# Optimization experiments

Hardware: AMD Instinct MI355X
Metric: run time of the kernel (lower is better)

Reference implementation:

```python
import jax, jax.numpy as jnp
import numpy as np

B, S, L = 2, 1024, 1024
DIM_Q, H, K, D_C, D_CQ, R = 2048, 16, 128, 512, 1536, 64


def _rope_tables(length, dim):
    # matches _RoPECache._build_tables: repeat_interleave(2) layout
    inv = 1.0 / (10000.0 ** (jnp.arange(0, dim, 2, dtype=jnp.float32) / dim))
    f = jnp.arange(length, dtype=jnp.float32)[:, None] * inv[None, :]  # [len, dim/2]
    sin = jnp.repeat(jnp.sin(f), 2, axis=-1)
    cos = jnp.repeat(jnp.cos(f), 2, axis=-1)
    return sin, cos


def _rotate_half(x):
    half = x.shape[-1] // 2
    return jnp.concatenate([-x[..., half:], x[..., :half]], axis=-1)


def _apply_rope(x, sin, cos):
    return x * cos + _rotate_half(x) * sin


def setup_inputs() -> dict:
    key = jax.random.key(0)
    ks = jax.random.split(key, 8)
    return {
        "hidden_q": jax.random.normal(ks[0], (B, S, DIM_Q), jnp.float32),
        "kv_c": jax.random.normal(ks[1], (B, L, D_C), jnp.float32),
        "Wq": jax.random.normal(ks[2], (H * K, DIM_Q), jnp.float32) / np.sqrt(DIM_Q).astype(np.float32),
        "w_kc_q": jax.random.normal(ks[3], (H, K, D_CQ), jnp.float32) / np.sqrt(K).astype(np.float32),
        "w_kc_kv": jax.random.normal(ks[4], (H, K, D_C), jnp.float32) / np.sqrt(K).astype(np.float32),
        "W_qr": jax.random.normal(ks[5], (H, D_CQ, R), jnp.float32) / np.float32(np.sqrt(D_CQ) * np.sqrt(R)),
        "W_kr": jax.random.normal(ks[6], (H, D_C, R), jnp.float32) / np.sqrt(D_C).astype(np.float32),
        "Wo": jax.random.normal(ks[7], (DIM_Q, H * K), jnp.float32) / np.sqrt(H * K).astype(np.float32),
    }


def reference(hidden_q, kv_c, Wq, w_kc_q, w_kc_kv, W_qr, W_kr, Wo):
    Bv, Sv, _ = hidden_q.shape
    _, Lv, _ = kv_c.shape
    # latent -> per-head queries, then decompress to d_cq
    q_hk = (hidden_q @ Wq.T).reshape(Bv, Sv, H, K)          # [B,S,H,K]
    q_big = jnp.einsum('bshk,hkq->bshq', q_hk, w_kc_q)      # [B,S,H,d_cq]
    sin_q, cos_q = _rope_tables(Sv, D_CQ)
    q_big = _apply_rope(q_big, sin_q[None, :, None, :], cos_q[None, :, None, :])
    sin_k, cos_k = _rope_tables(Lv, D_C)
    kv_r = _apply_rope(kv_c, sin_k[None], cos_k[None])      # [B,L,d_c]
    # retrieval projections (scale 1/sqrt(r) baked into W_qr)
    q_r = jnp.einsum('bshq,hqr->bhsr', q_big, W_qr)         # [B,H,S,r]
    k_r = jnp.einsum('bld,hdr->bhlr', kv_r, W_kr)           # [B,H,L,r]
    scores = jnp.einsum('bhsr,bhlr->bhsl', q_r, k_r)
    attn = jax.nn.softmax(scores, axis=-1)
    # values are the (RoPE'd) compressed kv shared across heads
    ctx_c = jnp.einsum('bhsl,bld->bhsd', attn, kv_r)        # [B,H,S,d_c]
    # decompress context: w_kc_kv.transpose(1,2) is [H,d_c,K]
    ctx_lat = jnp.einsum('bhsd,hkd->bhsk', ctx_c, w_kc_kv)  # [B,H,S,K]
    ctx = ctx_lat.transpose(0, 2, 1, 3).reshape(Bv, Sv, H * K)
    return ctx @ Wo.T
```

## Files before the change

kernel.cpp:

```cpp
#include <hip/hip_runtime.h>
#include <hip/hip_bf16.h>


typedef __attribute__((ext_vector_type(8))) short short8;
typedef __attribute__((ext_vector_type(4))) float f32x4;

__device__ __forceinline__ unsigned short f2bs(float v){
  __hip_bfloat16 b = __float2bfloat16(v);
  return *reinterpret_cast<unsigned short*>(&b);
}
__device__ __forceinline__ void storeC(float* p, float v){ *p = v; }
__device__ __forceinline__ void storeC(unsigned short* p, float v){ *p = f2bs(v); }

__device__ __forceinline__ void gl_lds16(const void* g, void* l){
  __builtin_amdgcn_global_load_lds(
      (const __attribute__((address_space(1))) unsigned int*)g,
      (__attribute__((address_space(3))) unsigned int*)l, 16, 0, 0);
}

template<int N> __device__ __forceinline__ void wait_vmcnt(){
  if constexpr (N==0)       asm volatile("s_waitcnt vmcnt(0)" ::: "memory");
  else if constexpr (N==3)  asm volatile("s_waitcnt vmcnt(3)" ::: "memory");
  else if constexpr (N==4)  asm volatile("s_waitcnt vmcnt(4)" ::: "memory");
  else if constexpr (N==6)  asm volatile("s_waitcnt vmcnt(6)" ::: "memory");
  else if constexpr (N==8)  asm volatile("s_waitcnt vmcnt(8)" ::: "memory");
  else if constexpr (N==14) asm volatile("s_waitcnt vmcnt(14)" ::: "memory");
  else if constexpr (N==16) asm volatile("s_waitcnt vmcnt(16)" ::: "memory");
  else if constexpr (N==22) asm volatile("s_waitcnt vmcnt(22)" ::: "memory");
  else static_assert(N==0, "unsupported vmcnt");
}

__device__ __forceinline__ void transpose_tile(
    const float* ip, unsigned short* op, int R, int Cn, int c0, int r0)
{
  __shared__ float tile[32][33];
  int tr = threadIdx.x>>5, tc = threadIdx.x&31;
  #pragma unroll
  for (int i=0;i<4;i++)
    tile[tr+i*8][tc] = ip[(long)(r0+tr+i*8)*Cn + c0+tc];
  __syncthreads();
  #pragma unroll
  for (int i=0;i<4;i++)
    op[(long)(c0+tr+i*8)*R + r0+tc] = f2bs(tile[tc][tr+i*8]);
}

__global__ __launch_bounds__(256) void prep_all(
    float4* __restrict__ rq,
    const float* __restrict__ kvc, unsigned short* __restrict__ kvrb,
    const float* __restrict__ hidden, unsigned short* __restrict__ hiddenb,
    const float* __restrict__ Wq, unsigned short* __restrict__ Wqb,
    const float* __restrict__ wkckv, unsigned short* __restrict__ wkckvb,
    const float* __restrict__ Wo, unsigned short* __restrict__ Wob,
    const float* __restrict__ wkcq, unsigned short* __restrict__ wkcqT,
    const float* __restrict__ Wqr, unsigned short* __restrict__ WqrT,
    const float* __restrict__ Wkr, unsigned short* __restrict__ WkrT)
{
  int blk = blockIdx.x;
  if (blk < 3072){
    int idx = blk*256 + threadIdx.x;
    int s = idx / 768, j = idx - (idx/768)*768;
    int i1 = j >> 1;
    const float cst = -0.011992631f;
    float f1 = (float)s * __expf(cst * (float)i1);
    float f2 = (float)s * __expf(cst * (float)(384 + i1));
    float s1, c1, s2, c2;
    __sincosf(f1, &s1, &c1);
    __sincosf(f2, &s2, &c2);
    rq[idx] = make_float4(c1, s1, c2, s2);
    return;
  }
  if (blk < 4096){
    int idx = (blk-3072)*256 + threadIdx.x;
    int i1 = idx & 127;
    int l  = (idx >> 7) & 1023;
    int bb = idx >> 17;
    const float cst = -0.035977892f;
    float f1 = (float)l * __expf(cst * (float)i1);
    float f2 = (float)l * __expf(cst * (float)(128 + i1));
    float s1,c1,s2,c2; __sincosf(f1,&s1,&c1); __sincosf(f2,&s2,&c2);
    long base = ((long)bb*1024 + l)*512;
    float2 xlo = *(const float2*)&kvc[base + 2*i1];
    float2 xhi = *(const float2*)&kvc[base + 2*i1 + 256];
    unsigned int lo = (unsigned)f2bs(xlo.x*c1 - xhi.x*s1)
                    | ((unsigned)f2bs(xlo.y*c1 - xhi.y*s1) << 16);
    unsigned int hi = (unsigned)f2bs(xhi.x*c2 + xlo.x*s2)
                    | ((unsigned)f2bs(xhi.y*c2 + xlo.y*s2) << 16);
    *(unsigned int*)&kvrb[base + 2*i1]       = lo;
    *(unsigned int*)&kvrb[base + 2*i1 + 256] = hi;
    return;
  }
  if (blk < 17408){
    const float* in; unsigned short* out; int i;
    if (blk < 8192){ in = hidden; out = hiddenb; i = (blk-4096)*256 + threadIdx.x; }
    else if (blk < 12288){ in = Wq; out = Wqb; i = (blk-8192)*256 + threadIdx.x; }
    else if (blk < 13312){ in = wkckv; out = wkckvb; i = (blk-12288)*256 + threadIdx.x; }
    else { in = Wo; out = Wob; i = (blk-13312)*256 + threadIdx.x; }
    float4 v = *(const float4*)(in + (long)i*4);
    ushort4 u; u.x=f2bs(v.x); u.y=f2bs(v.y); u.z=f2bs(v.z); u.w=f2bs(v.w);
    *(ushort4*)(out + (long)i*4) = u;
    return;
  }
  if (blk < 20480){
    int b2 = blk - 17408;
    int x = b2 % 48, rem = b2 / 48, y = rem % 4, z = rem >> 2;
    transpose_tile(wkcq + (long)z*196608, wkcqT + (long)z*196608,
                   128, 1536, x*32, y*32);
    return;
  }
  if (blk < 22016){
    int b2 = blk - 20480;
    int x = b2 & 1, rem = b2 >> 1, y = rem % 48, z = rem / 48;
    transpose_tile(Wqr + (long)z*98304, WqrT + (long)z*98304,
                   1536, 64, x*32, y*32);
    return;
  }
  {
    int b2 = blk - 22016;
    int x = b2 & 1, y = (b2 >> 1) & 15, z = b2 >> 5;
    transpose_tile(Wkr + (long)z*32768, WkrT + (long)z*32768,
                   512, 64, x*32, y*32);
  }
}

template<int BM,int BN,int WM,int WN,typename TC>
__global__ __launch_bounds__(256) void gemm_mfma(
    const unsigned short* __restrict__ A, const unsigned short* __restrict__ B,
    TC* __restrict__ C,
    int Kd, int lda, int ldb, int ldc, int Hb,
    long sAb, long sAh, long sBb, long sBh, long sCb, long sCh)
{
  constexpr int MF = WM/16, NF = WN/16;
  constexpr int WGM = BM/WM;
  constexpr int AOPS = (4*BM)/256;
  constexpr int BOPS = (4*BN)/256;
  constexpr int STG  = AOPS + BOPS;

  const int z = blockIdx.z, bb = z/Hb, hh = z - bb*Hb;
  const unsigned short* Ap = A + bb*sAb + hh*sAh;
  const unsigned short* Bp = B + bb*sBb + hh*sBh;
  TC* Cp = C + bb*sCb + hh*sCh;
  const int m0 = blockIdx.x*BM, n0 = blockIdx.y*BN;
  const int t = threadIdx.x, w = t>>6, l = t&63;
  const int wm0 = (w % WGM)*WM, wn0 = (w / WGM)*WN;
  const int lq = l>>4, lm = l&15;

  __shared__ __align__(16) unsigned short As[4][4*BM*8];
  __shared__ __align__(16) unsigned short Bs[4][4*BN*8];

  f32x4 acc[MF][NF];
  #pragma unroll
  for (int mf=0; mf<MF; ++mf)
    #pragma unroll
    for (int nf=0; nf<NF; ++nf)
      acc[mf][nf] = f32x4{0.f,0.f,0.f,0.f};

  auto stage = [&](int buf, int k0){
    #pragma unroll
    for (int o = 0; o < AOPS; ++o){
      int g = o*256 + t;
      int row = g & (BM-1), kq = g / BM;
      gl_lds16(Ap + (long)(m0+row)*lda + k0 + kq*8, &As[buf][(o*256 + w*64)*8]);
    }
    #pragma unroll
    for (int o = 0; o < BOPS; ++o){
      int g = o*256 + t;
      int row = g & (BN-1), kq = g / BN;
      gl_lds16(Bp + (long)(n0+row)*ldb + k0 + kq*8, &Bs[buf][(o*256 + w*64)*8]);
    }
  };

  const int nIter = Kd >> 5;
  stage(0, 0);
  if (1 < nIter) stage(1, 32);
  if (2 < nIter) stage(2, 64);

  for (int it = 0; it < nIter; ++it){
    const int cur = it & 3;
    const int rem = nIter - it;
    if (rem >= 3)      wait_vmcnt<2*STG>();
    else if (rem == 2) wait_vmcnt<STG>();
    else               wait_vmcnt<0>();
    __builtin_amdgcn_s_barrier();

    short8 af[MF], bfr[NF];
    #pragma unroll
    for (int mf=0; mf<MF; ++mf)
      af[mf] = *(const short8*)&As[cur][(lq*BM + wm0 + mf*16 + lm)*8];
    #pragma unroll
    for (int nf=0; nf<NF; ++nf)
      bfr[nf] = *(const short8*)&Bs[cur][(lq*BN + wn0 + nf*16 + lm)*8];
    #pragma unroll
    for (int mf=0; mf<MF; ++mf)
      #pragma unroll
      for (int nf=0; nf<NF; ++nf)
        acc[mf][nf] = __builtin_amdgcn_mfma_f32_16x16x32_bf16(
            af[mf], bfr[nf], acc[mf][nf], 0, 0, 0);

    if (it+3 < nIter) stage((it+3) & 3, (it+3)*32);
  }

  #pragma unroll
  for (int mf=0; mf<MF; ++mf){
    #pragma unroll
    for (int nf=0; nf<NF; ++nf){
      int row = m0 + wm0 + mf*16 + lq*4;
      int col = n0 + wn0 + nf*16 + lm;
      #pragma unroll
      for (int r=0; r<4; ++r)
        storeC(&Cp[(long)(row+r)*ldc + col], acc[mf][nf][r]);
    }
  }
}

__global__ __launch_bounds__(256) void q_fused(
    const unsigned short* __restrict__ A,
    const unsigned short* __restrict__ W1t,
    const unsigned short* __restrict__ W2t,
    const float4* __restrict__ rq,
    unsigned short* __restrict__ qrOut)
{
  const int z = blockIdx.z, bb = z>>4, hh = z&15;
  const int m0 = blockIdx.x*64;
  const unsigned short* Ap = A + (long)bb*2097152 + hh*128;
  const unsigned short* W1 = W1t + (long)hh*196608;
  const unsigned short* W2 = W2t + (long)hh*98304;
  unsigned short* qo = qrOut + ((long)z*1024 + m0)*64;

  const int t = threadIdx.x, w = t>>6, l = t&63;
  const int lq = l>>4, lm = l&15;
  const int wr = (w>>1)*32;
  const int wc = w&1;

  __shared__ __align__(16) unsigned short W1s[2][16*64*8];
  __shared__ __align__(16) unsigned short W2s[2][8*64*8];
  __shared__ __align__(16) unsigned short Ps[64*72];

  short8 af[2][4];
  #pragma unroll
  for (int mf=0; mf<2; ++mf)
    #pragma unroll
    for (int ks=0; ks<4; ++ks)
      af[mf][ks] = *(const short8*)&Ap[(long)(m0 + wr + mf*16 + lm)*2048 + (ks*4+lq)*8];

  auto stageW = [&](int buf, int cn){
    #pragma unroll
    for (int o=0;o<4;++o){
      int g=o*256+t; int row=g&63, kq=g>>6;
      int grow = (row<32) ? (cn*32+row) : (736+cn*32+row);
      gl_lds16(W1 + (long)grow*128 + kq*8, &W1s[buf][(o*256+w*64)*8]);
    }
    #pragma unroll
    for (int o=0;o<2;++o){
      int g=o*256+t; int n=g&63, kq=g>>6;
      int qk = (kq<4) ? (cn*32+kq*8) : (736+cn*32+kq*8);
      gl_lds16(W2 + (long)n*1536 + qk, &W2s[buf][(o*256+w*64)*8]);
    }
  };
  stageW(0, 0);

  f32x4 accr[2][2];
  #pragma unroll
  for (int mf=0; mf<2; ++mf)
    #pragma unroll
    for (int nf=0; nf<2; ++nf) accr[mf][nf] = f32x4{0.f,0.f,0.f,0.f};

  for (int cn = 0; cn < 24; ++cn){
    const int cur = cn & 1;

    float4 rc_reg[2][4];
    #pragma unroll
    for (int mf=0; mf<2; ++mf)
      #pragma unroll
      for (int r=0; r<4; ++r){
        int srow = m0 + wr + mf*16 + lq*4 + r;
        rc_reg[mf][r] = rq[(long)srow*768 + cn*32 + wc*16 + lm];
      }
    if (cn < 23) stageW(cur^1, cn+1);
    if (cn < 23) wait_vmcnt<14>(); else wait_vmcnt<8>();
    __builtin_amdgcn_s_barrier();

    f32x4 sa[2][2];
    #pragma unroll
    for (int mf=0; mf<2; ++mf)
      #pragma unroll
      for (int p=0; p<2; ++p) sa[mf][p] = f32x4{0.f,0.f,0.f,0.f};
    #pragma unroll
    for (int ks=0; ks<4; ++ks){
      short8 blo = *(const short8*)&W1s[cur][((ks*4+lq)*64 + wc*16 + lm)*8];
      short8 bhi = *(const short8*)&W1s[cur][((ks*4+lq)*64 + 32 + wc*16 + lm)*8];
      sa[0][0] = __builtin_amdgcn_mfma_f32_16x16x32_bf16(af[0][ks], blo, sa[0][0], 0,0,0);
      sa[0][1] = __builtin_amdgcn_mfma_f32_16x16x32_bf16(af[0][ks], bhi, sa[0][1], 0,0,0);
      sa[1][0] = __builtin_amdgcn_mfma_f32_16x16x32_bf16(af[1][ks], blo, sa[1][0], 0,0,0);
      sa[1][1] = __builtin_amdgcn_mfma_f32_16x16x32_bf16(af[1][ks], bhi, sa[1][1], 0,0,0);
    }

    #pragma unroll
    for (int mf=0; mf<2; ++mf)
      #pragma unroll
      for (int r=0; r<4; ++r){
        int prow = wr + mf*16 + lq*4 + r;
        float4 rc = rc_reg[mf][r];
        float xl = sa[mf][0][r], xh = sa[mf][1][r];
        Ps[prow*72 + wc*16 + lm]      = f2bs(xl*rc.x - xh*rc.y);
        Ps[prow*72 + 32 + wc*16 + lm] = f2bs(xh*rc.z + xl*rc.w);
      }
    asm volatile("s_waitcnt lgkmcnt(0)" ::: "memory");
    __builtin_amdgcn_sched_barrier(0);
    __builtin_amdgcn_s_barrier();

    #pragma unroll
    for (int ks=0; ks<2; ++ks){
      short8 ap0 = *(const short8*)&Ps[(wr + lm)*72 + ks*32 + lq*8];
      short8 ap1 = *(const short8*)&Ps[(wr + 16 + lm)*72 + ks*32 + lq*8];
      #pragma unroll
      for (int nf=0; nf<2; ++nf){
        short8 bw = *(const short8*)&W2s[cur][((ks*4+lq)*64 + wc*32 + nf*16 + lm)*8];
        accr[0][nf] = __builtin_amdgcn_mfma_f32_16x16x32_bf16(ap0, bw, accr[0][nf], 0,0,0);
        accr[1][nf] = __builtin_amdgcn_mfma_f32_16x16x32_bf16(ap1, bw, accr[1][nf], 0,0,0);
      }
    }
    __builtin_amdgcn_s_barrier();
  }

  #pragma unroll
  for (int mf=0; mf<2; ++mf)
    #pragma unroll
    for (int nf=0; nf<2; ++nf)
      #pragma unroll
      for (int r=0; r<4; ++r)
        qo[(long)(wr + mf*16 + lq*4 + r)*64 + wc*32 + nf*16 + lm] = f2bs(accr[mf][nf][r]);
}

__global__ __launch_bounds__(256) void flash_mfma(
    const unsigned short* __restrict__ qr, const unsigned short* __restrict__ kr,
    const unsigned short* __restrict__ vt, unsigned short* __restrict__ ctx)
{
  const int b = blockIdx.z, h = blockIdx.y, s0 = blockIdx.x*64;
  const int t = threadIdx.x, w = t>>6, l = t&63;
  const int lq = l>>4, lm = l&15;

  __shared__ __align__(16) unsigned short Qs[8*64*8];
  __shared__ __align__(16) unsigned short Ks[2][8*64*8];
  __shared__ __align__(16) unsigned short Vts[2][8*128*8];
  __shared__ __align__(16) unsigned short Ps[64*72];

  const unsigned short* qbase = qr + ((long)(b*16+h)*1024 + s0)*64;
  const unsigned short* kbase = kr + (long)(b*16+h)*65536;
  const unsigned short* vbase = vt + (long)(b*16+h)*131072;

  auto stageKV = [&](int buf, int l0){
    #pragma unroll
    for (int o = 0; o < 2; ++o){
      int g = o*256 + t;
      int row = g & 63, kq = g >> 6;
      gl_lds16(kbase + (long)(l0+row)*64 + kq*8, &Ks[buf][(o*256 + w*64)*8]);
    }
    #pragma unroll
    for (int o = 0; o < 4; ++o){
      int g = o*256 + t;
      int row = g & 127, kq = g >> 7;
      gl_lds16(vbase + (long)row*1024 + l0 + kq*8, &Vts[buf][(o*256 + w*64)*8]);
    }
  };

  #pragma unroll
  for (int o = 0; o < 2; ++o){
    int g = o*256 + t;
    int row = g & 63, kq = g >> 6;
    gl_lds16(qbase + (long)row*64 + kq*8, &Qs[(o*256 + w*64)*8]);
  }
  stageKV(0, 0);
  __syncthreads();
  short8 aq[2];
  #pragma unroll
  for (int ks = 0; ks < 2; ++ks)
    aq[ks] = *(const short8*)&Qs[((ks*4+lq)*64 + w*16 + lm)*8];

  float m_run[4], l_run[4];
  #pragma unroll
  for (int r = 0; r < 4; ++r){ m_run[r] = -3e38f; l_run[r] = 0.f; }
  f32x4 acc_o[8];
  #pragma unroll
  for (int nf = 0; nf < 8; ++nf) acc_o[nf] = f32x4{0.f,0.f,0.f,0.f};

  for (int it = 0; it < 16; ++it){
    const int cur = it & 1;
    if (it < 15){ stageKV(cur^1, (it+1)*64); wait_vmcnt<6>(); }
    else        { wait_vmcnt<0>(); }
    __builtin_amdgcn_s_barrier();

    f32x4 acc_s[4];
    #pragma unroll
    for (int nf = 0; nf < 4; ++nf) acc_s[nf] = f32x4{0.f,0.f,0.f,0.f};
    #pragma unroll
    for (int ks = 0; ks < 2; ++ks)
      #pragma unroll
      for (int nf = 0; nf < 4; ++nf){
        short8 bf = *(const short8*)&Ks[cur][((ks*4+lq)*64 + nf*16 + lm)*8];
        acc_s[nf] = __builtin_amdgcn_mfma_f32_16x16x32_bf16(
            aq[ks], bf, acc_s[nf], 0, 0, 0);
      }

    float tmax[4];
    #pragma unroll
    for (int r = 0; r < 4; ++r)
      tmax[r] = fmaxf(fmaxf(acc_s[0][r], acc_s[1][r]),
                      fmaxf(acc_s[2][r], acc_s[3][r]));
    #pragma unroll
    for (int mask = 1; mask < 16; mask <<= 1)
      #pragma unroll
      for (int r = 0; r < 4; ++r)
        tmax[r] = fmaxf(tmax[r], __shfl_xor(tmax[r], mask));
    float alpha[4], rsum[4];
    #pragma unroll
    for (int r = 0; r < 4; ++r){
      float mnew = fmaxf(m_run[r], tmax[r]);
      alpha[r] = __expf(m_run[r] - mnew);
      m_run[r] = mnew;
      rsum[r] = 0.f;
    }
    #pragma unroll
    for (int nf = 0; nf < 4; ++nf)
      #pragma unroll
      for (int r = 0; r < 4; ++r){
        float p = __expf(acc_s[nf][r] - m_run[r]);
        rsum[r] += p;
        Ps[(w*16 + lq*4 + r)*72 + nf*16 + lm] = f2bs(p);
      }
    #pragma unroll
    for (int mask = 1; mask < 16; mask <<= 1)
      #pragma unroll
      for (int r = 0; r < 4; ++r)
        rsum[r] += __shfl_xor(rsum[r], mask);
    #pragma unroll
    for (int r = 0; r < 4; ++r)
      l_run[r] = l_run[r]*alpha[r] + rsum[r];

    #pragma unroll
    for (int nf = 0; nf < 8; ++nf)
      #pragma unroll
      for (int r = 0; r < 4; ++r)
        acc_o[nf][r] *= alpha[r];

    short8 ap[2];
    #pragma unroll
    for (int ks = 0; ks < 2; ++ks)
      ap[ks] = *(const short8*)&Ps[(w*16 + lm)*72 + ks*32 + lq*8];
    #pragma unroll
    for (int ks = 0; ks < 2; ++ks)
      #pragma unroll
      for (int nf = 0; nf < 8; ++nf){
        short8 bv = *(const short8*)&Vts[cur][((ks*4+lq)*128 + nf*16 + lm)*8];
        acc_o[nf] = __builtin_amdgcn_mfma_f32_16x16x32_bf16(
            ap[ks], bv, acc_o[nf], 0, 0, 0);
      }
    __builtin_amdgcn_s_barrier();
  }

  float inv[4];
  #pragma unroll
  for (int r = 0; r < 4; ++r) inv[r] = 1.f / l_run[r];
  #pragma unroll
  for (int nf = 0; nf < 8; ++nf)
    #pragma unroll
    for (int r = 0; r < 4; ++r){
      long row = (long)b*1024 + s0 + w*16 + lq*4 + r;
      ctx[row*2048 + h*128 + nf*16 + lm] = f2bs(acc_o[nf][r]*inv[r]);
    }
}

extern "C" void kernel_launch(void* const* d_in, const int* in_sizes, int n_in,
                              void* d_out, int out_size, void* d_ws, size_t ws_size,
                              hipStream_t stream)
{
  const float* hidden_q = (const float*)d_in[0];
  const float* kv_c     = (const float*)d_in[1];
  const float* Wq       = (const float*)d_in[2];
  const float* w_kc_q   = (const float*)d_in[3];
  const float* w_kc_kv  = (const float*)d_in[4];
  const float* W_qr     = (const float*)d_in[5];
  const float* W_kr     = (const float*)d_in[6];
  const float* Wo       = (const float*)d_in[7];
  float* out = (float*)d_out;

  char* wsb = (char*)d_ws;
  size_t off = 0;
  auto take = [&](size_t bytes)->void*{
    void* p = wsb + off; off += (bytes + 255) & ~(size_t)255; return p;
  };
  unsigned short* q_rb  = (unsigned short*)take(4194304);
  unsigned short* k_rb  = (unsigned short*)take(4194304);
  unsigned short* kv_rb = (unsigned short*)take(2097152);
  float4* ropeq4 = (float4*)take(12582912);
  unsigned short* q_hk   = (unsigned short*)take(8388608);
  unsigned short* wkcqT  = (unsigned short*)take(6291456);
  unsigned short* WqrT   = (unsigned short*)take(3145728);
  unsigned short* wkckvb = (unsigned short*)take(2097152);
  unsigned short* WkrT   = (unsigned short*)take(1048576);
  unsigned short* Vt     = (unsigned short*)take(8388608);
  unsigned short* hiddenb = (unsigned short*)take(8388608);
  unsigned short* Wqb     = (unsigned short*)take(8388608);
  unsigned short* Wob     = (unsigned short*)take(8388608);
  unsigned short* ctx_lat = (unsigned short*)take(8388608);

  prep_all<<<22528, 256, 0, stream>>>(ropeq4,
      kv_c, kv_rb,
      hidden_q, hiddenb, Wq, Wqb, w_kc_kv, wkckvb, Wo, Wob,
      w_kc_q, wkcqT, W_qr, WqrT, W_kr, WkrT);

  gemm_mfma<128,128,64,64,unsigned short><<<dim3(16,16,1),256,0,stream>>>(
      hiddenb, Wqb, q_hk, 2048, 2048,2048,2048, 1, 0,0, 0,0, 0,0);

  q_fused<<<dim3(16,1,32),256,0,stream>>>(q_hk, wkcqT, WqrT, ropeq4, q_rb);

  gemm_mfma<128,64,64,32,unsigned short><<<dim3(8,1,32),256,0,stream>>>(
      kv_rb, WkrT, k_rb, 512, 512,512,64, 16,
      524288,0, 0,32768, 1048576,65536);

  gemm_mfma<128,128,64,64,unsigned short><<<dim3(1,8,32),256,0,stream>>>(
      wkckvb, kv_rb, Vt, 512, 512,512,1024, 16,
      0,65536, 524288,0, 2097152,131072);

  flash_mfma<<<dim3(16,16,2),256,0,stream>>>(q_rb, k_rb, Vt, ctx_lat);

  gemm_mfma<128,128,64,64,float><<<dim3(16,16,1),256,0,stream>>>(
      ctx_lat, Wob, out, 2048, 2048,2048,2048, 1, 0,0, 0,0, 0,0);
}
```

Measured before the change: 333.6 us.

## Load W1 into registers and split-K second GEMM per warp with LDS reduction

The fused q-rope-retrieval kernel now loads W1 fragments straight from global memory into double-buffered registers instead of staging them in LDS. Each warp writes its rotated P tile to a private LDS slice, so the block-wide barrier between the rope step and the second GEMM goes away. Each warp now accumulates a K-split of the full 64-column output, and the two column-warps are reduced through LDS at the end. This cuts LDS traffic and barriers in exchange for more VGPR pressure, duplicated W1 global reads across row-warps, and a final reduction step.

Measured after the change: 350.7 us. 1.05x slower.

```diff
diff --git a/kernel.cpp b/kernel.cpp
--- a/kernel.cpp
+++ b/kernel.cpp
@@ -231,9 +231,9 @@
   const int wr = (w>>1)*32;
   const int wc = w&1;
 
-  __shared__ __align__(16) unsigned short W1s[2][16*64*8];
   __shared__ __align__(16) unsigned short W2s[2][8*64*8];
-  __shared__ __align__(16) unsigned short Ps[64*72];
+  __shared__ __align__(16) unsigned short Pp[4][32*36];
+  __shared__ float Fred[2][32][64];
 
   short8 af[2][4];
   #pragma unroll
@@ -242,13 +242,14 @@
     for (int ks=0; ks<4; ++ks)
       af[mf][ks] = *(const short8*)&Ap[(long)(m0 + wr + mf*16 + lm)*2048 + (ks*4+lq)*8];
 
-  auto stageW = [&](int buf, int cn){
-    #pragma unroll
-    for (int o=0;o<4;++o){
-      int g=o*256+t; int row=g&63, kq=g>>6;
-      int grow = (row<32) ? (cn*32+row) : (736+cn*32+row);
-      gl_lds16(W1 + (long)grow*128 + kq*8, &W1s[buf][(o*256+w*64)*8]);
-    }
+  auto loadW1 = [&](short8 (&dst)[8], int cn){
+    #pragma unroll
+    for (int ks=0; ks<4; ++ks){
+      dst[ks*2]   = *(const short8*)&W1[(long)(cn*32 + wc*16 + lm)*128 + (ks*4+lq)*8];
+      dst[ks*2+1] = *(const short8*)&W1[(long)(768 + cn*32 + wc*16 + lm)*128 + (ks*4+lq)*8];
+    }
+  };
+  auto stageW2 = [&](int buf, int cn){
     #pragma unroll
     for (int o=0;o<2;++o){
       int g=o*256+t; int n=g&63, kq=g>>6;
@@ -256,79 +257,95 @@
       gl_lds16(W2 + (long)n*1536 + qk, &W2s[buf][(o*256+w*64)*8]);
     }
   };
-  stageW(0, 0);
-
-  f32x4 accr[2][2];
+
+  short8 w1a[8], w1b[8];
+  loadW1(w1a, 0);
+  stageW2(0, 0);
+
+  f32x4 accr[2][4];
   #pragma unroll
   for (int mf=0; mf<2; ++mf)
     #pragma unroll
-    for (int nf=0; nf<2; ++nf) accr[mf][nf] = f32x4{0.f,0.f,0.f,0.f};
-
-  for (int cn = 0; cn < 24; ++cn){
+    for (int nf=0; nf<4; ++nf) accr[mf][nf] = f32x4{0.f,0.f,0.f,0.f};
+
+  auto body = [&](int cn, short8 (&w1c)[8], short8 (&w1n)[8]){
     const int cur = cn & 1;
-
     float4 rc_reg[2][4];
     #pragma unroll
     for (int mf=0; mf<2; ++mf)
       #pragma unroll
+      for (int r=0; r<4; ++r)
+        rc_reg[mf][r] = rq[(long)(m0 + wr + mf*16 + lq*4 + r)*768 + cn*32 + wc*16 + lm];
+    if (cn < 23) loadW1(w1n, cn+1);
+    if (cn < 23) wait_vmcnt<16>(); else wait_vmcnt<8>();
+    __builtin_amdgcn_s_barrier();
+    if (cn < 23) stageW2(cur^1, cn+1);
+
+    f32x4 sa[2][2];
+    #pragma unroll
+    for (int mf=0; mf<2; ++mf)
+      #pragma unroll
+      for (int p=0; p<2; ++p) sa[mf][p] = f32x4{0.f,0.f,0.f,0.f};
+    #pragma unroll
+    for (int ks=0; ks<4; ++ks){
+      sa[0][0] = __builtin_amdgcn_mfma_f32_16x16x32_bf16(af[0][ks], w1c[ks*2],   sa[0][0], 0,0,0);
+      sa[0][1] = __builtin_amdgcn_mfma_f32_16x16x32_bf16(af[0][ks], w1c[ks*2+1], sa[0][1], 0,0,0);
+      sa[1][0] = __builtin_amdgcn_mfma_f32_16x16x32_bf16(af[1][ks], w1c[ks*2],   sa[1][0], 0,0,0);
+      sa[1][1] = __builtin_amdgcn_mfma_f32_16x16x32_bf16(af[1][ks], w1c[ks*2+1], sa[1][1], 0,0,0);
+    }
+
+    #pragma unroll
+    for (int mf=0; mf<2; ++mf)
+      #pragma unroll
       for (int r=0; r<4; ++r){
-        int srow = m0 + wr + mf*16 + lq*4 + r;
-        rc_reg[mf][r] = rq[(long)srow*768 + cn*32 + wc*16 + lm];
-      }
-    if (cn < 23) stageW(cur^1, cn+1);
-    if (cn < 23) wait_vmcnt<14>(); else wait_vmcnt<8>();
-    __builtin_amdgcn_s_barrier();
-
-    f32x4 sa[2][2];
-    #pragma unroll
-    for (int mf=0; mf<2; ++mf)
-      #pragma unroll
-      for (int p=0; p<2; ++p) sa[mf][p] = f32x4{0.f,0.f,0.f,0.f};
-    #pragma unroll
-    for (int ks=0; ks<4; ++ks){
-      short8 blo = *(const short8*)&W1s[cur][((ks*4+lq)*64 + wc*16 + lm)*8];
-      short8 bhi = *(const short8*)&W1s[cur][((ks*4+lq)*64 + 32 + wc*16 + lm)*8];
-      sa[0][0] = __builtin_amdgcn_mfma_f32_16x16x32_bf16(af[0][ks], blo, sa[0][0], 0,0,0);
-      sa[0][1] = __builtin_amdgcn_mfma_f32_16x16x32_bf16(af[0][ks], bhi, sa[0][1], 0,0,0);
-      sa[1][0] = __builtin_amdgcn_mfma_f32_16x16x32_bf16(af[1][ks], blo, sa[1][0], 0,0,0);
-      sa[1][1] = __builtin_amdgcn_mfma_f32_16x16x32_bf16(af[1][ks], bhi, sa[1][1], 0,0,0);
-    }
-
-    #pragma unroll
-    for (int mf=0; mf<2; ++mf)
-      #pragma unroll
-      for (int r=0; r<4; ++r){
-        int prow = wr + mf*16 + lq*4 + r;
+        int prow = mf*16 + lq*4 + r;
         float4 rc = rc_reg[mf][r];
         float xl = sa[mf][0][r], xh = sa[mf][1][r];
-        Ps[prow*72 + wc*16 + lm]      = f2bs(xl*rc.x - xh*rc.y);
-        Ps[prow*72 + 32 + wc*16 + lm] = f2bs(xh*rc.z + xl*rc.w);
+        Pp[w][prow*36 + lm]      = f2bs(xl*rc.x - xh*rc.y);
+        Pp[w][prow*36 + 16 + lm] = f2bs(xh*rc.z + xl*rc.w);
       }
     asm volatile("s_waitcnt lgkmcnt(0)" ::: "memory");
     __builtin_amdgcn_sched_barrier(0);
-    __builtin_amdgcn_s_barrier();
-
-    #pragma unroll
-    for (int ks=0; ks<2; ++ks){
-      short8 ap0 = *(const short8*)&Ps[(wr + lm)*72 + ks*32 + lq*8];
-      short8 ap1 = *(const short8*)&Ps[(wr + 16 + lm)*72 + ks*32 + lq*8];
-      #pragma unroll
-      for (int nf=0; nf<2; ++nf){
-        short8 bw = *(const short8*)&W2s[cur][((ks*4+lq)*64 + wc*32 + nf*16 + lm)*8];
-        accr[0][nf] = __builtin_amdgcn_mfma_f32_16x16x32_bf16(ap0, bw, accr[0][nf], 0,0,0);
-        accr[1][nf] = __builtin_amdgcn_mfma_f32_16x16x32_bf16(ap1, bw, accr[1][nf], 0,0,0);
-      }
-    }
-    __builtin_amdgcn_s_barrier();
-  }
-
-  #pragma unroll
-  for (int mf=0; mf<2; ++mf)
-    #pragma unroll
-    for (int nf=0; nf<2; ++nf)
-      #pragma unroll
-      for (int r=0; r<4; ++r)
-        qo[(long)(wr + mf*16 + lq*4 + r)*64 + wc*32 + nf*16 + lm] = f2bs(accr[mf][nf][r]);
+
+    short8 ap[2];
+    #pragma unroll
+    for (int mf=0; mf<2; ++mf)
+      ap[mf] = *(const short8*)&Pp[w][(mf*16 + lm)*36 + lq*8];
+    const int kqsel = 2*wc + lq + ((lq>>1)<<1);
+    #pragma unroll
+    for (int nf=0; nf<4; ++nf){
+      short8 bw = *(const short8*)&W2s[cur][(kqsel*64 + nf*16 + lm)*8];
+      accr[0][nf] = __builtin_amdgcn_mfma_f32_16x16x32_bf16(ap[0], bw, accr[0][nf], 0,0,0);
+      accr[1][nf] = __builtin_amdgcn_mfma_f32_16x16x32_bf16(ap[1], bw, accr[1][nf], 0,0,0);
+    }
+  };
+
+  for (int cn = 0; cn < 24; cn += 2){
+    body(cn,   w1a, w1b);
+    body(cn+1, w1b, w1a);
+  }
+
+  if (wc == 1){
+    #pragma unroll
+    for (int mf=0; mf<2; ++mf)
+      #pragma unroll
+      for (int nf=0; nf<4; ++nf)
+        #pragma unroll
+        for (int r=0; r<4; ++r)
+          Fred[w>>1][mf*16 + lq*4 + r][nf*16 + lm] = accr[mf][nf][r];
+  }
+  __syncthreads();
+  if (wc == 0){
+    #pragma unroll
+    for (int mf=0; mf<2; ++mf)
+      #pragma unroll
+      for (int nf=0; nf<4; ++nf)
+        #pragma unroll
+        for (int r=0; r<4; ++r){
+          float v = accr[mf][nf][r] + Fred[w>>1][mf*16 + lq*4 + r][nf*16 + lm];
+          qo[(long)(wr + mf*16 + lq*4 + r)*64 + nf*16 + lm] = f2bs(v);
+        }
+  }
 }
 
 __global__ __launch_bounds__(256) void flash_mfma(
```

## Merge Q projection, K-retrieval and V-transpose GEMMs into one launch

Applied to the files above, without the earlier changes.

Adds a grouped GEMM kernel that dispatches three independent GEMMs (hidden@Wq, kv_r@W_kr, w_kc_kv@kv_r) from one flat 640-block grid, replacing three separate launches. The K-retrieval GEMM now runs as a single wide 128x128 tile over all heads, which makes its output layout [B,L,H*R], so the flash kernel's K addressing is changed to match. This removes launch gaps and tail underutilisation for the two small GEMMs, which can now fill the GPU alongside the large one. The cost is one uniform tile config for all three and a strided K load in the attention kernel.

New measurement: 320.9 us. 3.8% less time.

```diff
diff --git a/kernel.cpp b/kernel.cpp
--- a/kernel.cpp
+++ b/kernel.cpp
@@ -212,6 +212,102 @@
   }
 }
 
+struct GP {
+  const unsigned short* A; const unsigned short* B; unsigned short* C;
+  int Kd, lda, ldb, ldc, Hb, gx, gy;
+  long sAb, sAh, sBb, sBh, sCb, sCh;
+};
+
+__global__ __launch_bounds__(256) void gemm_merged(GP g0, GP g1, GP g2,
+                                                   int n0b, int n1b)
+{
+  GP p; int rid;
+  {
+    int id = blockIdx.x;
+    if (id < n0b){ p = g0; rid = id; }
+    else if (id < n0b + n1b){ p = g1; rid = id - n0b; }
+    else { p = g2; rid = id - n0b - n1b; }
+  }
+  int bx = rid % p.gx; rid /= p.gx;
+  int by = rid % p.gy; int z = rid / p.gy;
+  const int bb = z / p.Hb, hh = z - bb*p.Hb;
+
+  const unsigned short* Ap = p.A + bb*p.sAb + hh*p.sAh;
+  const unsigned short* Bp = p.B + bb*p.sBb + hh*p.sBh;
+  unsigned short* Cp = p.C + bb*p.sCb + hh*p.sCh;
+  const int m0 = bx*128, n0 = by*128;
+  const int t = threadIdx.x, w = t>>6, l = t&63;
+  const int wm0 = (w & 1)*64, wn0 = (w >> 1)*64;
+  const int lq = l>>4, lm = l&15;
+
+  __shared__ __align__(16) unsigned short As[4][4*128*8];
+  __shared__ __align__(16) unsigned short Bs[4][4*128*8];
+
+  f32x4 acc[4][4];
+  #pragma unroll
+  for (int mf=0; mf<4; ++mf)
+    #pragma unroll
+    for (int nf=0; nf<4; ++nf)
+      acc[mf][nf] = f32x4{0.f,0.f,0.f,0.f};
+
+  auto stage = [&](int buf, int k0){
+    #pragma unroll
+    for (int o = 0; o < 2; ++o){
+      int g = o*256 + t;
+      int row = g & 127, kq = g >> 7;
+      gl_lds16(Ap + (long)(m0+row)*p.lda + k0 + kq*8, &As[buf][(o*256 + w*64)*8]);
+    }
+    #pragma unroll
+    for (int o = 0; o < 2; ++o){
+      int g = o*256 + t;
+      int row = g & 127, kq = g >> 7;
+      gl_lds16(Bp + (long)(n0+row)*p.ldb + k0 + kq*8, &Bs[buf][(o*256 + w*64)*8]);
+    }
+  };
+
+  const int nIter = p.Kd >> 5;
+  stage(0, 0);
+  if (1 < nIter) stage(1, 32);
+  if (2 < nIter) stage(2, 64);
+
+  for (int it = 0; it < nIter; ++it){
+    const int cur = it & 3;
+    const int rem = nIter - it;
+    if (rem >= 3)      wait_vmcnt<8>();
+    else if (rem == 2) wait_vmcnt<4>();
+    else               wait_vmcnt<0>();
+    __builtin_amdgcn_s_barrier();
+
+    short8 af[4], bfr[4];
+    #pragma unroll
+    for (int mf=0; mf<4; ++mf)
+      af[mf] = *(const short8*)&As[cur][(lq*128 + wm0 + mf*16 + lm)*8];
+    #pragma unroll
+    for (int nf=0; nf<4; ++nf)
+      bfr[nf] = *(const short8*)&Bs[cur][(lq*128 + wn0 + nf*16 + lm)*8];
+    #pragma unroll
+    for (int mf=0; mf<4; ++mf)
+      #pragma unroll
+      for (int nf=0; nf<4; ++nf)
+        acc[mf][nf] = __builtin_amdgcn_mfma_f32_16x16x32_bf16(
+            af[mf], bfr[nf], acc[mf][nf], 0, 0, 0);
+
+    if (it+3 < nIter) stage((it+3) & 3, (it+3)*32);
+  }
+
+  #pragma unroll
+  for (int mf=0; mf<4; ++mf){
+    #pragma unroll
+    for (int nf=0; nf<4; ++nf){
+      int row = m0 + wm0 + mf*16 + lq*4;
+      int col = n0 + wn0 + nf*16 + lm;
+      #pragma unroll
+      for (int r=0; r<4; ++r)
+        Cp[(long)(row+r)*p.ldc + col] = f2bs(acc[mf][nf][r]);
+    }
+  }
+}
+
 __global__ __launch_bounds__(256) void q_fused(
     const unsigned short* __restrict__ A,
     const unsigned short* __restrict__ W1t,
@@ -345,7 +441,7 @@
   __shared__ __align__(16) unsigned short Ps[64*72];
 
   const unsigned short* qbase = qr + ((long)(b*16+h)*1024 + s0)*64;
-  const unsigned short* kbase = kr + (long)(b*16+h)*65536;
+  const unsigned short* kbase = kr + (long)b*1048576 + h*64;
   const unsigned short* vbase = vt + (long)(b*16+h)*131072;
 
   auto stageKV = [&](int buf, int l0){
@@ -353,7 +449,7 @@
     for (int o = 0; o < 2; ++o){
       int g = o*256 + t;
       int row = g & 63, kq = g >> 6;
-      gl_lds16(kbase + (long)(l0+row)*64 + kq*8, &Ks[buf][(o*256 + w*64)*8]);
+      gl_lds16(kbase + (long)(l0+row)*1024 + kq*8, &Ks[buf][(o*256 + w*64)*8]);
     }
     #pragma unroll
     for (int o = 0; o < 4; ++o){
@@ -508,18 +604,12 @@
       hidden_q, hiddenb, Wq, Wqb, w_kc_kv, wkckvb, Wo, Wob,
       w_kc_q, wkcqT, W_qr, WqrT, W_kr, WkrT);
 
-  gemm_mfma<128,128,64,64,unsigned short><<<dim3(16,16,1),256,0,stream>>>(
-      hiddenb, Wqb, q_hk, 2048, 2048,2048,2048, 1, 0,0, 0,0, 0,0);
+  GP g0{hiddenb, Wqb, q_hk,   2048, 2048, 2048, 2048, 1, 16, 16, 0, 0, 0, 0, 0, 0};
+  GP g1{kv_rb,  WkrT, k_rb,    512,  512,  512, 1024, 1,  8,  8, 524288, 0, 0, 0, 1048576, 0};
+  GP g2{wkckvb, kv_rb, Vt,     512,  512,  512, 1024, 16, 1,  8, 0, 65536, 524288, 0, 2097152, 131072};
+  gemm_merged<<<640, 256, 0, stream>>>(g0, g1, g2, 256, 128);
 
   q_fused<<<dim3(16,1,32),256,0,stream>>>(q_hk, wkcqT, WqrT, ropeq4, q_rb);
-
-  gemm_mfma<128,64,64,32,unsigned short><<<dim3(8,1,32),256,0,stream>>>(
-      kv_rb, WkrT, k_rb, 512, 512,512,64, 16,
-      524288,0, 0,32768, 1048576,65536);
-
-  gemm_mfma<128,128,64,64,unsigned short><<<dim3(1,8,32),256,0,stream>>>(
-      wkckvb, kv_rb, Vt, 512, 512,512,1024, 16,
-      0,65536, 524288,0, 2097152,131072);
 
   flash_mfma<<<dim3(16,16,2),256,0,stream>>>(q_rb, k_rb, Vt, ctx_lat);
 
```
